# Optimization experiments

Measured on AMD Instinct MI355X. Metric: run time of the kernel, lower is better.

## Reference

```python
import jax, jax.numpy as jnp
import numpy as np

EPS = 1e-5

def setup_inputs() -> dict:
    key = jax.random.key(0)
    ks = jax.random.split(key, 10)
    B, N, D = 1, 20000, 256
    E, H = 320000, 8
    s = 1.0 / np.sqrt(D)
    return {
        "node_embeddings": jax.random.normal(ks[0], (B, N, D), jnp.float32),
        "edge_index": jax.random.randint(ks[1], (2, E), 0, N, jnp.int32),
        "edge_weights": jax.random.uniform(ks[2], (E,), jnp.float32),
        "Wq": jax.random.normal(ks[3], (D, D), jnp.float32) * s,
        "Wk": jax.random.normal(ks[4], (D, D), jnp.float32) * s,
        "Wv": jax.random.normal(ks[5], (D, D), jnp.float32) * s,
        "We": jax.random.normal(ks[6], (H,), jnp.float32),  # edge_encoder weight [num_heads,1] squeezed
        "Wo": jax.random.normal(ks[7], (D, D), jnp.float32) * s,
        "ln_g": jnp.ones((D,), jnp.float32),
        "ln_b": jnp.zeros((D,), jnp.float32),
    }

def reference(node_embeddings, edge_index, edge_weights, Wq, Wk, Wv, We, Wo, ln_g, ln_b):
    B, N, D = node_embeddings.shape
    H = We.shape[0]
    hd = D // H
    scale = 1.0 / np.sqrt(hd)
    residual = node_embeddings

    # projections -> [B, N, H, hd]
    Q = (node_embeddings @ Wq).reshape(B, N, H, hd)
    K = (node_embeddings @ Wk).reshape(B, N, H, hd)
    V = (node_embeddings @ Wv).reshape(B, N, H, hd)

    src = edge_index[0]
    tgt = edge_index[1]
    E = src.shape[0]

    # gather per edge, edge axis leading for segment ops: [E, B, H, hd]
    Q_e = jnp.moveaxis(Q[:, src], 1, 0)
    K_e = jnp.moveaxis(K[:, tgt], 1, 0)
    V_e = jnp.moveaxis(V[:, tgt], 1, 0)

    # per-edge scores [E, B, H]
    scores = (Q_e * K_e).sum(-1) * scale
    bias = edge_weights[:, None] * We[None, :]            # [E, H]
    scores = scores + bias[:, None, :]

    # scatter softmax grouped by source node
    m = jax.ops.segment_max(scores, src, num_segments=N)   # [N, B, H]
    p = jnp.exp(scores - m[src])
    denom = jax.ops.segment_sum(p, src, num_segments=N)    # [N, B, H]
    attn = p / denom[src]                                   # [E, B, H]

    # scatter-add weighted V -> [N, B, H, hd]
    weighted = attn[..., None] * V_e
    agg = jax.ops.segment_sum(weighted.reshape(E, -1), src, num_segments=N)
    agg = agg.reshape(N, B, H, hd)

    attn_out = jnp.moveaxis(agg, 0, 1).reshape(B, N, D)     # [B, N, D]
    out = attn_out @ Wo

    x = out + residual
    mu = x.mean(-1, keepdims=True)
    var = ((x - mu) ** 2).mean(-1, keepdims=True)
    return (x - mu) / jnp.sqrt(var + EPS) * ln_g + ln_b
```

## Files before the change

kernel.cpp:

```cpp
#include <hip/hip_runtime.h>
#include <hip/hip_bf16.h>

typedef __attribute__((ext_vector_type(8))) short short8;
typedef __attribute__((ext_vector_type(4))) short short4_t;
typedef __attribute__((ext_vector_type(4))) float f32x4;

#define CH 64

__device__ __forceinline__ ushort f2b(float f) {
  __hip_bfloat16 h = __float2bfloat16(f);
  return *reinterpret_cast<ushort*>(&h);
}
__device__ __forceinline__ float b2f(ushort u) {
  return __uint_as_float(((unsigned)u) << 16);
}
__device__ __forceinline__ void wave_lds_sync() {
  asm volatile("s_waitcnt lgkmcnt(0)" ::: "memory");
  __builtin_amdgcn_wave_barrier();
}

__global__ __launch_bounds__(256) void pre_kernel(
    const float* __restrict__ X, ushort* __restrict__ Xb, int nX,
    const float* __restrict__ Wq, const float* __restrict__ Wk,
    const float* __restrict__ Wv, const float* __restrict__ Wo,
    ushort* __restrict__ Wt, int* __restrict__ counts, int N, int nxb) {
  __shared__ float L[32][33];
  int b = blockIdx.x;
  int t = threadIdx.x;
  if (b < nxb) {
    int i = (b * 256 + t) * 8;
    if (i >= nX) return;
    float4 x0 = *reinterpret_cast<const float4*>(X + i);
    float4 x1 = *reinterpret_cast<const float4*>(X + i + 4);
    short8 o;
    o[0] = (short)f2b(x0.x); o[1] = (short)f2b(x0.y);
    o[2] = (short)f2b(x0.z); o[3] = (short)f2b(x0.w);
    o[4] = (short)f2b(x1.x); o[5] = (short)f2b(x1.y);
    o[6] = (short)f2b(x1.z); o[7] = (short)f2b(x1.w);
    *reinterpret_cast<short8*>(Xb + i) = o;
  } else if (b < nxb + 256) {
    int bx = b - nxb;
    int mat = bx >> 6;
    int tile = bx & 63;
    int tr = (tile >> 3) * 32;
    int tc = (tile & 7) * 32;
    const float* W = (mat == 0) ? Wq : (mat == 1) ? Wk : (mat == 2) ? Wv : Wo;
    int c = t & 31, r8 = t >> 5;
#pragma unroll
    for (int rr = 0; rr < 4; ++rr) {
      int r = r8 + rr * 8;
      L[r][c] = W[(size_t)(tr + r) * 256 + tc + c];
    }
    __syncthreads();
#pragma unroll
    for (int rr = 0; rr < 4; ++rr) {
      int cc = r8 + rr * 8;
      Wt[(size_t)(mat * 256 + tc + cc) * 256 + tr + c] = f2b(L[c][cc]);
    }
  } else {
    int i = (b - nxb - 256) * 256 + t;
    if (i < N) counts[i] = 0;
  }
}

__global__ __launch_bounds__(256) void hist_gemm(
    const ushort* __restrict__ Xb, const ushort* __restrict__ Wt,
    ushort* __restrict__ QKVb, const int* __restrict__ src,
    int* __restrict__ counts, int N, int E, int ngemm) {
  __shared__ ushort sA[128 * 64];
  __shared__ ushort sB[128 * 64];
  int bid = blockIdx.x;
  int t = threadIdx.x;
  if (bid >= ngemm) {
    int e = (bid - ngemm) * 256 + t;
    if (e < E) atomicAdd(&counts[src[e]], 1);
    return;
  }
  int bx = bid / 6, by = bid % 6;
  char* cA = (char*)sA;
  char* cB = (char*)sB;
  int lane = t & 63, w = t >> 6;
  int wr = w >> 1, wc = w & 1;
  int row0 = bx * 128;
  int lr = lane & 15, kg = lane >> 4;
  f32x4 acc[4][4] = {};
  for (int k0 = 0; k0 < 256; k0 += 64) {
#pragma unroll
    for (int it = 0; it < 4; ++it) {
      int slot = t + it * 256;
      int row = slot >> 3, kc = slot & 7;
      int grow = min(row0 + row, N - 1);
      short8 va = *reinterpret_cast<const short8*>(Xb + (size_t)grow * 256 + k0 + kc * 8);
      *reinterpret_cast<short8*>(cA + ((row * 128 + kc * 16) ^ ((row & 7) << 4))) = va;
      short8 vb = *reinterpret_cast<const short8*>(Wt + (size_t)(by * 128 + row) * 256 + k0 + kc * 8);
      *reinterpret_cast<short8*>(cB + ((row * 128 + kc * 16) ^ ((row & 7) << 4))) = vb;
    }
    __syncthreads();
#pragma unroll
    for (int ks = 0; ks < 2; ++ks) {
      short8 af[4], bf[4];
#pragma unroll
      for (int fr = 0; fr < 4; ++fr) {
        int row = wr * 64 + fr * 16 + lr;
        af[fr] = *reinterpret_cast<const short8*>(
            cA + ((row * 128 + ks * 64 + kg * 16) ^ ((row & 7) << 4)));
      }
#pragma unroll
      for (int fc = 0; fc < 4; ++fc) {
        int col = wc * 64 + fc * 16 + lr;
        bf[fc] = *reinterpret_cast<const short8*>(
            cB + ((col * 128 + ks * 64 + kg * 16) ^ ((col & 7) << 4)));
      }
#pragma unroll
      for (int fr = 0; fr < 4; ++fr)
#pragma unroll
        for (int fc = 0; fc < 4; ++fc)
          acc[fr][fc] = __builtin_amdgcn_mfma_f32_16x16x32_bf16(af[fr], bf[fc], acc[fr][fc], 0, 0, 0);
    }
    __syncthreads();
  }
  int orow = kg * 4;
#pragma unroll
  for (int fr = 0; fr < 4; ++fr)
#pragma unroll
    for (int fc = 0; fc < 4; ++fc)
#pragma unroll
      for (int r = 0; r < 4; ++r) {
        int row = row0 + wr * 64 + fr * 16 + orow + r;
        int col = by * 128 + wc * 64 + fc * 16 + lr;
        if (row < N) QKVb[(size_t)row * 768 + col] = f2b(acc[fr][fc][r]);
      }
}

__global__ __launch_bounds__(1024) void scan_kernel(
    const int* __restrict__ counts, int* __restrict__ offs, int* __restrict__ cursor, int N) {
  __shared__ int wsum[16];
  __shared__ int wexc[16];
  __shared__ int s_total;
  int t = threadIdx.x;
  int lane = t & 63, wv = t >> 6;
  int per = (N + 1023) >> 10;
  int b0 = t * per;
  int e0 = min(b0 + per, N);
  int sum = 0;
  for (int i = b0; i < e0; ++i) sum += counts[i];
  int x = sum;
#pragma unroll
  for (int off = 1; off < 64; off <<= 1) {
    int y = __shfl_up(x, off);
    if (lane >= off) x += y;
  }
  if (lane == 63) wsum[wv] = x;
  __syncthreads();
  if (t < 64) {
    int s = (lane < 16) ? wsum[lane] : 0;
    int xs = s;
#pragma unroll
    for (int off = 1; off < 16; off <<= 1) {
      int y = __shfl_up(xs, off);
      if (lane >= off) xs += y;
    }
    if (lane < 16) wexc[lane] = xs - s;
    if (lane == 15) s_total = xs;
  }
  __syncthreads();
  int running = wexc[wv] + (x - sum);
  for (int i = b0; i < e0; ++i) {
    int c = counts[i];
    offs[i] = running;
    cursor[i] = running;
    running += c;
  }
  if (t == 0) offs[N] = s_total;
}

__global__ void scatter_kernel(const int* __restrict__ src, const int* __restrict__ tgt,
                               const float* __restrict__ ew, int* __restrict__ cursor,
                               int* __restrict__ tgt_s, float* __restrict__ w_s, int E) {
  int e = blockIdx.x * blockDim.x + threadIdx.x;
  if (e < E) {
    int pos = atomicAdd(&cursor[src[e]], 1);
    tgt_s[pos] = tgt[e];
    w_s[pos] = ew[e];
  }
}

__global__ __launch_bounds__(256) void attn_kernel(
    const ushort* __restrict__ QKVb,
    const int* __restrict__ offs, const int* __restrict__ tgt_s, const float* __restrict__ w_s,
    const float* __restrict__ We, ushort* __restrict__ AGGb, int N) {
  __shared__ float s_p[4][CH][8];
  __shared__ int s_tgt[4][CH];
  __shared__ float s_w[4][CH];
  int t = threadIdx.x;
  int w = t >> 6;
  int l = t & 63;
  int i = blockIdx.x * 4 + w;
  if (i >= N) return;
  int e8 = l >> 3;
  int h = l & 7;
  int hacc = l >> 3;
  const float scale = 0.17677669529663687f;
  float we = We[h];

  float qf[32];
  {
    const short8* qr = reinterpret_cast<const short8*>(QKVb + (size_t)i * 768 + h * 32);
#pragma unroll
    for (int d = 0; d < 4; ++d) {
      short8 qv = qr[d];
#pragma unroll
      for (int x = 0; x < 8; ++x) qf[d * 8 + x] = b2f((ushort)qv[x]);
    }
  }

  float m = -1e30f, lsum = 0.f;
  float acc0 = 0.f, acc1 = 0.f, acc2 = 0.f, acc3 = 0.f;
  int beg = offs[i], end = offs[i + 1];

  for (int base = beg; base < end; base += CH) {
    int cnt = min(CH, end - base);
    int cnt_pad = (cnt + 7) & ~7;
    {
      bool valid = l < cnt;
      int tg = valid ? tgt_s[base + l] : i;
      float ww = valid ? w_s[base + l] : 0.f;
      s_tgt[w][l] = tg;
      s_w[w][l] = ww;
    }
    wave_lds_sync();

    short8 kc[4], kn[4];
    {
      const short8* p = reinterpret_cast<const short8*>(
          QKVb + (size_t)s_tgt[w][e8] * 768 + 256 + h * 32);
#pragma unroll
      for (int d = 0; d < 4; ++d) kc[d] = p[d];
    }
    if (8 < cnt_pad) {
      const short8* p = reinterpret_cast<const short8*>(
          QKVb + (size_t)s_tgt[w][8 + e8] * 768 + 256 + h * 32);
#pragma unroll
      for (int d = 0; d < 4; ++d) kn[d] = p[d];
    }
    short4_t vc[8], vn[8];
#pragma unroll
    for (int k = 0; k < 8; ++k)
      vc[k] = *reinterpret_cast<const short4_t*>(
          QKVb + (size_t)s_tgt[w][k] * 768 + 512 + l * 4);
    if (8 < cnt_pad) {
#pragma unroll
      for (int k = 0; k < 8; ++k)
        vn[k] = *reinterpret_cast<const short4_t*>(
            QKVb + (size_t)s_tgt[w][8 + k] * 768 + 512 + l * 4);
    }

    float s_local[8];
#pragma unroll
    for (int it = 0; it < 8; ++it) s_local[it] = -1e30f;
    float cmax = -1e30f;
#pragma unroll
    for (int it = 0; it < 8; ++it) {
      if (it * 8 >= cnt_pad) break;
      float dot = 0.f;
#pragma unroll
      for (int d = 0; d < 4; ++d)
#pragma unroll
        for (int x = 0; x < 8; ++x)
          dot += qf[d * 8 + x] * b2f((ushort)kc[d][x]);
      int j = it * 8 + e8;
      float s = (j < cnt) ? dot * scale + s_w[w][j] * we : -1e30f;
      s_local[it] = s;
      cmax = fmaxf(cmax, s);
#pragma unroll
      for (int d = 0; d < 4; ++d) kc[d] = kn[d];
      if ((it + 2) * 8 < cnt_pad) {
        const short8* p = reinterpret_cast<const short8*>(
            QKVb + (size_t)s_tgt[w][(it + 2) * 8 + e8] * 768 + 256 + h * 32);
#pragma unroll
        for (int d = 0; d < 4; ++d) kn[d] = p[d];
      }
    }
    cmax = fmaxf(cmax, __shfl_xor(cmax, 8));
    cmax = fmaxf(cmax, __shfl_xor(cmax, 16));
    cmax = fmaxf(cmax, __shfl_xor(cmax, 32));
    float newm = fmaxf(m, cmax);
    float f = __expf(m - newm);
    float psum = 0.f;
#pragma unroll
    for (int it = 0; it < 8; ++it) {
      if (it * 8 >= cnt_pad) break;
      int j = it * 8 + e8;
      float p = __expf(s_local[it] - newm);
      s_p[w][j][h] = p;
      psum += p;
    }
    psum += __shfl_xor(psum, 8);
    psum += __shfl_xor(psum, 16);
    psum += __shfl_xor(psum, 32);
    lsum = lsum * f + psum;
    m = newm;
    float f_acc = __shfl(f, hacc);
    acc0 *= f_acc; acc1 *= f_acc; acc2 *= f_acc; acc3 *= f_acc;
    wave_lds_sync();

#pragma unroll
    for (int g = 0; g < 8; ++g) {
      if (g * 8 >= cnt_pad) break;
      float pv[8];
#pragma unroll
      for (int k = 0; k < 8; ++k) pv[k] = s_p[w][g * 8 + k][hacc];
#pragma unroll
      for (int k = 0; k < 8; ++k) {
        acc0 += pv[k] * b2f((ushort)vc[k][0]);
        acc1 += pv[k] * b2f((ushort)vc[k][1]);
        acc2 += pv[k] * b2f((ushort)vc[k][2]);
        acc3 += pv[k] * b2f((ushort)vc[k][3]);
      }
#pragma unroll
      for (int k = 0; k < 8; ++k) vc[k] = vn[k];
      if ((g + 2) * 8 < cnt_pad) {
#pragma unroll
        for (int k = 0; k < 8; ++k)
          vn[k] = *reinterpret_cast<const short4_t*>(
              QKVb + (size_t)s_tgt[w][(g + 2) * 8 + k] * 768 + 512 + l * 4);
      }
    }
    wave_lds_sync();
  }
  float lsum_acc = __shfl(lsum, hacc);
  float rinv = (lsum_acc > 0.f) ? 1.f / lsum_acc : 0.f;
  short4_t o;
  o[0] = (short)f2b(acc0 * rinv);
  o[1] = (short)f2b(acc1 * rinv);
  o[2] = (short)f2b(acc2 * rinv);
  o[3] = (short)f2b(acc3 * rinv);
  *reinterpret_cast<short4_t*>(AGGb + (size_t)i * 256 + l * 4) = o;
}

__global__ __launch_bounds__(256) void out_ln(
    const ushort* __restrict__ AGGb, const ushort* __restrict__ Wot,
    const float* __restrict__ X, const float* __restrict__ g, const float* __restrict__ bb,
    float* __restrict__ out, int N) {
  __shared__ ushort sA[64 * 64];
  __shared__ ushort sB[256 * 64];
  char* cA = (char*)sA;
  char* cB = (char*)sB;
  int t = threadIdx.x;
  int lane = t & 63, w = t >> 6;
  int row0 = blockIdx.x * 64;
  int lr = lane & 15, kg = lane >> 4;
  f32x4 acc[16] = {};
  for (int k0 = 0; k0 < 256; k0 += 64) {
#pragma unroll
    for (int it = 0; it < 2; ++it) {
      int slot = t + it * 256;
      int row = slot >> 3, kc = slot & 7;
      int grow = min(row0 + row, N - 1);
      short8 va = *reinterpret_cast<const short8*>(AGGb + (size_t)grow * 256 + k0 + kc * 8);
      *reinterpret_cast<short8*>(cA + ((row * 128 + kc * 16) ^ ((row & 7) << 4))) = va;
    }
#pragma unroll
    for (int it = 0; it < 8; ++it) {
      int slot = t + it * 256;
      int col = slot >> 3, kc = slot & 7;
      short8 vb = *reinterpret_cast<const short8*>(Wot + (size_t)col * 256 + k0 + kc * 8);
      *reinterpret_cast<short8*>(cB + ((col * 128 + kc * 16) ^ ((col & 7) << 4))) = vb;
    }
    __syncthreads();
#pragma unroll
    for (int ks = 0; ks < 2; ++ks) {
      int arow = w * 16 + lr;
      short8 a = *reinterpret_cast<const short8*>(
          cA + ((arow * 128 + ks * 64 + kg * 16) ^ ((arow & 7) << 4)));
#pragma unroll
      for (int fc = 0; fc < 16; ++fc) {
        int col = fc * 16 + lr;
        short8 b = *reinterpret_cast<const short8*>(
            cB + ((col * 128 + ks * 64 + kg * 16) ^ ((col & 7) << 4)));
        acc[fc] = __builtin_amdgcn_mfma_f32_16x16x32_bf16(a, b, acc[fc], 0, 0, 0);
      }
    }
    __syncthreads();
  }
  float g16[16], b16[16];
#pragma unroll
  for (int fc = 0; fc < 16; ++fc) {
    g16[fc] = g[fc * 16 + lr];
    b16[fc] = bb[fc * 16 + lr];
  }
#pragma unroll
  for (int r = 0; r < 4; ++r) {
    int rowl = kg * 4 + r;
    int grow = row0 + w * 16 + rowl;
    int growc = min(grow, N - 1);
    float xv[16];
    float s = 0.f, ss = 0.f;
#pragma unroll
    for (int fc = 0; fc < 16; ++fc) {
      float v = acc[fc][r] + X[(size_t)growc * 256 + fc * 16 + lr];
      xv[fc] = v;
      s += v;
      ss += v * v;
    }
    s += __shfl_xor(s, 1);  ss += __shfl_xor(ss, 1);
    s += __shfl_xor(s, 2);  ss += __shfl_xor(ss, 2);
    s += __shfl_xor(s, 4);  ss += __shfl_xor(ss, 4);
    s += __shfl_xor(s, 8);  ss += __shfl_xor(ss, 8);
    float mu = s * (1.f / 256.f);
    float var = ss * (1.f / 256.f) - mu * mu;
    float rs = rsqrtf(var + 1e-5f);
    if (grow < N) {
#pragma unroll
      for (int fc = 0; fc < 16; ++fc)
        out[(size_t)grow * 256 + fc * 16 + lr] = (xv[fc] - mu) * rs * g16[fc] + b16[fc];
    }
  }
}

extern "C" void kernel_launch(void* const* d_in, const int* in_sizes, int n_in,
                              void* d_out, int out_size, void* d_ws, size_t ws_size,
                              hipStream_t stream) {
  const float* X  = (const float*)d_in[0];
  const int* eidx = (const int*)d_in[1];
  const float* ew = (const float*)d_in[2];
  const float* Wq = (const float*)d_in[3];
  const float* Wk = (const float*)d_in[4];
  const float* Wv = (const float*)d_in[5];
  const float* We = (const float*)d_in[6];
  const float* Wo = (const float*)d_in[7];
  const float* g  = (const float*)d_in[8];
  const float* b  = (const float*)d_in[9];
  int N = in_sizes[0] / 256;
  int E = in_sizes[1] / 2;
  const int* src = eidx;
  const int* tgt = eidx + E;
  float* out = (float*)d_out;

  char* w = (char*)d_ws;
  ushort* Xb   = (ushort*)w;  w += (size_t)N * 256 * 2;
  ushort* Wt   = (ushort*)w;  w += (size_t)1024 * 256 * 2;
  ushort* QKVb = (ushort*)w;  w += (size_t)N * 768 * 2;
  ushort* AGGb = (ushort*)w;  w += (size_t)N * 256 * 2;
  int* counts  = (int*)w;     w += (size_t)N * 4;
  int* offs    = (int*)w;     w += (size_t)(N + 1) * 4;
  int* cursor  = (int*)w;     w += (size_t)N * 4;
  int* tgt_s   = (int*)w;     w += (size_t)E * 4;
  float* w_s   = (float*)w;   w += (size_t)E * 4;
  const ushort* Wot = Wt + (size_t)768 * 256;

  int nX = N * 256;
  int nxb = (nX / 8 + 255) / 256;
  int nzero = (N + 255) / 256;
  pre_kernel<<<nxb + 256 + nzero, 256, 0, stream>>>(X, Xb, nX, Wq, Wk, Wv, Wo, Wt, counts, N, nxb);

  int ngemm = ((N + 127) / 128) * 6;
  int nhist = (E + 255) / 256;
  hist_gemm<<<ngemm + nhist, 256, 0, stream>>>(Xb, Wt, QKVb, src, counts, N, E, ngemm);

  scan_kernel<<<1, 1024, 0, stream>>>(counts, offs, cursor, N);
  scatter_kernel<<<(E + 255) / 256, 256, 0, stream>>>(src, tgt, ew, cursor, tgt_s, w_s, E);
  attn_kernel<<<(N + 3) / 4, 256, 0, stream>>>(QKVb, offs, tgt_s, w_s, We, AGGb, N);
  out_ln<<<(N + 63) / 64, 256, 0, stream>>>(AGGb, Wot, X, g, b, out, N);
}
```

Baseline: 167.1 us.

## Fuse X bf16 conversion into QKV GEMM; defer V loads and raise wave priority

Removes the separate X-to-bf16 conversion pass and its intermediate buffer: the QKV GEMM now loads fp32 X directly and converts while staging into shared memory. This saves a full write and read of the bf16 copy, but the GEMM reads twice the bytes for A and repeats the conversion once per column block (6 times). In the attention kernel, V loads are moved after the score loop to cut register pressure during the K phase. The per-chunk work is also wrapped in s_setprio to raise wave priority.

```diff
diff --git a/kernel.cpp b/kernel.cpp
--- a/kernel.cpp
+++ b/kernel.cpp
@@ -20,28 +20,15 @@
 }
 
 __global__ __launch_bounds__(256) void pre_kernel(
-    const float* __restrict__ X, ushort* __restrict__ Xb, int nX,
     const float* __restrict__ Wq, const float* __restrict__ Wk,
     const float* __restrict__ Wv, const float* __restrict__ Wo,
-    ushort* __restrict__ Wt, int* __restrict__ counts, int N, int nxb) {
+    ushort* __restrict__ Wt, int* __restrict__ counts, int N) {
   __shared__ float L[32][33];
   int b = blockIdx.x;
   int t = threadIdx.x;
-  if (b < nxb) {
-    int i = (b * 256 + t) * 8;
-    if (i >= nX) return;
-    float4 x0 = *reinterpret_cast<const float4*>(X + i);
-    float4 x1 = *reinterpret_cast<const float4*>(X + i + 4);
-    short8 o;
-    o[0] = (short)f2b(x0.x); o[1] = (short)f2b(x0.y);
-    o[2] = (short)f2b(x0.z); o[3] = (short)f2b(x0.w);
-    o[4] = (short)f2b(x1.x); o[5] = (short)f2b(x1.y);
-    o[6] = (short)f2b(x1.z); o[7] = (short)f2b(x1.w);
-    *reinterpret_cast<short8*>(Xb + i) = o;
-  } else if (b < nxb + 256) {
-    int bx = b - nxb;
-    int mat = bx >> 6;
-    int tile = bx & 63;
+  if (b < 256) {
+    int mat = b >> 6;
+    int tile = b & 63;
     int tr = (tile >> 3) * 32;
     int tc = (tile & 7) * 32;
     const float* W = (mat == 0) ? Wq : (mat == 1) ? Wk : (mat == 2) ? Wv : Wo;
@@ -58,13 +45,13 @@
       Wt[(size_t)(mat * 256 + tc + cc) * 256 + tr + c] = f2b(L[c][cc]);
     }
   } else {
-    int i = (b - nxb - 256) * 256 + t;
+    int i = (b - 256) * 256 + t;
     if (i < N) counts[i] = 0;
   }
 }
 
 __global__ __launch_bounds__(256) void hist_gemm(
-    const ushort* __restrict__ Xb, const ushort* __restrict__ Wt,
+    const float* __restrict__ X, const ushort* __restrict__ Wt,
     ushort* __restrict__ QKVb, const int* __restrict__ src,
     int* __restrict__ counts, int N, int E, int ngemm) {
   __shared__ ushort sA[128 * 64];
@@ -90,7 +77,14 @@
       int slot = t + it * 256;
       int row = slot >> 3, kc = slot & 7;
       int grow = min(row0 + row, N - 1);
-      short8 va = *reinterpret_cast<const short8*>(Xb + (size_t)grow * 256 + k0 + kc * 8);
+      const float* xp = X + (size_t)grow * 256 + k0 + kc * 8;
+      float4 x0 = *reinterpret_cast<const float4*>(xp);
+      float4 x1 = *reinterpret_cast<const float4*>(xp + 4);
+      short8 va;
+      va[0] = (short)f2b(x0.x); va[1] = (short)f2b(x0.y);
+      va[2] = (short)f2b(x0.z); va[3] = (short)f2b(x0.w);
+      va[4] = (short)f2b(x1.x); va[5] = (short)f2b(x1.y);
+      va[6] = (short)f2b(x1.z); va[7] = (short)f2b(x1.w);
       *reinterpret_cast<short8*>(cA + ((row * 128 + kc * 16) ^ ((row & 7) << 4))) = va;
       short8 vb = *reinterpret_cast<const short8*>(Wt + (size_t)(by * 128 + row) * 256 + k0 + kc * 8);
       *reinterpret_cast<short8*>(cB + ((row * 128 + kc * 16) ^ ((row & 7) << 4))) = vb;
@@ -230,6 +224,7 @@
     }
     wave_lds_sync();
 
+    __builtin_amdgcn_s_setprio(1);
     short8 kc[4], kn[4];
     {
       const short8* p = reinterpret_cast<const short8*>(
@@ -242,17 +237,6 @@
           QKVb + (size_t)s_tgt[w][8 + e8] * 768 + 256 + h * 32);
 #pragma unroll
       for (int d = 0; d < 4; ++d) kn[d] = p[d];
-    }
-    short4_t vc[8], vn[8];
-#pragma unroll
-    for (int k = 0; k < 8; ++k)
-      vc[k] = *reinterpret_cast<const short4_t*>(
-          QKVb + (size_t)s_tgt[w][k] * 768 + 512 + l * 4);
-    if (8 < cnt_pad) {
-#pragma unroll
-      for (int k = 0; k < 8; ++k)
-        vn[k] = *reinterpret_cast<const short4_t*>(
-            QKVb + (size_t)s_tgt[w][8 + k] * 768 + 512 + l * 4);
     }
 
     float s_local[8];
@@ -281,6 +265,19 @@
         for (int d = 0; d < 4; ++d) kn[d] = p[d];
       }
     }
+
+    short4_t vc[8], vn[8];
+#pragma unroll
+    for (int k = 0; k < 8; ++k)
+      vc[k] = *reinterpret_cast<const short4_t*>(
+          QKVb + (size_t)s_tgt[w][k] * 768 + 512 + l * 4);
+    if (8 < cnt_pad) {
+#pragma unroll
+      for (int k = 0; k < 8; ++k)
+        vn[k] = *reinterpret_cast<const short4_t*>(
+            QKVb + (size_t)s_tgt[w][8 + k] * 768 + 512 + l * 4);
+    }
+
     cmax = fmaxf(cmax, __shfl_xor(cmax, 8));
     cmax = fmaxf(cmax, __shfl_xor(cmax, 16));
     cmax = fmaxf(cmax, __shfl_xor(cmax, 32));
@@ -326,6 +323,7 @@
               QKVb + (size_t)s_tgt[w][(g + 2) * 8 + k] * 768 + 512 + l * 4);
       }
     }
+    __builtin_amdgcn_s_setprio(0);
     wave_lds_sync();
   }
   float lsum_acc = __shfl(lsum, hacc);
@@ -438,7 +436,6 @@
   float* out = (float*)d_out;
 
   char* w = (char*)d_ws;
-  ushort* Xb   = (ushort*)w;  w += (size_t)N * 256 * 2;
   ushort* Wt   = (ushort*)w;  w += (size_t)1024 * 256 * 2;
   ushort* QKVb = (ushort*)w;  w += (size_t)N * 768 * 2;
   ushort* AGGb = (ushort*)w;  w += (size_t)N * 256 * 2;
@@ -449,14 +446,12 @@
   float* w_s   = (float*)w;   w += (size_t)E * 4;
   const ushort* Wot = Wt + (size_t)768 * 256;
 
-  int nX = N * 256;
-  int nxb = (nX / 8 + 255) / 256;
   int nzero = (N + 255) / 256;
-  pre_kernel<<<nxb + 256 + nzero, 256, 0, stream>>>(X, Xb, nX, Wq, Wk, Wv, Wo, Wt, counts, N, nxb);
+  pre_kernel<<<256 + nzero, 256, 0, stream>>>(Wq, Wk, Wv, Wo, Wt, counts, N);
 
   int ngemm = ((N + 127) / 128) * 6;
   int nhist = (E + 255) / 256;
-  hist_gemm<<<ngemm + nhist, 256, 0, stream>>>(Xb, Wt, QKVb, src, counts, N, E, ngemm);
+  hist_gemm<<<ngemm + nhist, 256, 0, stream>>>(X, Wt, QKVb, src, counts, N, E, ngemm);
 
   scan_kernel<<<1, 1024, 0, stream>>>(counts, offs, cursor, N);
   scatter_kernel<<<(E + 255) / 256, 256, 0, stream>>>(src, tgt, ew, cursor, tgt_s, w_s, E);
```

After: 169.7 us. No clear change (+1.6%).

## Store K and V in FP8 and pack edge target/weight into int2

Applied to the files above, without the earlier changes.

The QKV projection now writes Q as bf16 and K and V as FP8 e4m3 in separate buffers. This halves the bytes the attention kernel gathers per edge for keys and values. The scatter step packs each edge's target and weight into one int2, and the GEMM block index is remapped across XCDs for locality. The V prefetch double-buffering is dropped in favour of direct loads, and FP8 quantization of K/V adds precision loss.

```diff
diff --git a/kernel.cpp b/kernel.cpp
--- a/kernel.cpp
+++ b/kernel.cpp
@@ -1,8 +1,9 @@
 #include <hip/hip_runtime.h>
 #include <hip/hip_bf16.h>
+#include <hip/hip_fp8.h>
 
 typedef __attribute__((ext_vector_type(8))) short short8;
-typedef __attribute__((ext_vector_type(4))) short short4_t;
+typedef __attribute__((ext_vector_type(16))) unsigned char uchar16;
 typedef __attribute__((ext_vector_type(4))) float f32x4;
 
 #define CH 64
@@ -13,6 +14,15 @@
 }
 __device__ __forceinline__ float b2f(ushort u) {
   return __uint_as_float(((unsigned)u) << 16);
+}
+__device__ __forceinline__ unsigned char f2e4(float f) {
+  __hip_fp8_e4m3 h(f);
+  return *reinterpret_cast<unsigned char*>(&h);
+}
+__device__ __forceinline__ float e42f(unsigned char u) {
+  __hip_fp8_e4m3 h;
+  *reinterpret_cast<unsigned char*>(&h) = u;
+  return (float)h;
 }
 __device__ __forceinline__ void wave_lds_sync() {
   asm volatile("s_waitcnt lgkmcnt(0)" ::: "memory");
@@ -63,9 +73,10 @@
   }
 }
 
-__global__ __launch_bounds__(256) void hist_gemm(
+__global__ __launch_bounds__(256) void gemm_hist(
     const ushort* __restrict__ Xb, const ushort* __restrict__ Wt,
-    ushort* __restrict__ QKVb, const int* __restrict__ src,
+    ushort* __restrict__ Qb, unsigned char* __restrict__ Kb8,
+    unsigned char* __restrict__ Vb8, const int* __restrict__ src,
     int* __restrict__ counts, int N, int E, int ngemm) {
   __shared__ ushort sA[128 * 64];
   __shared__ ushort sB[128 * 64];
@@ -76,7 +87,10 @@
     if (e < E) atomicAdd(&counts[src[e]], 1);
     return;
   }
-  int bx = bid / 6, by = bid % 6;
+  int q = ngemm >> 3, r = ngemm & 7;
+  int xcd = bid & 7;
+  int wgid = (xcd < r ? xcd * (q + 1) : r * (q + 1) + (xcd - r) * q) + (bid >> 3);
+  int bx = wgid / 6, by = wgid % 6;
   char* cA = (char*)sA;
   char* cB = (char*)sB;
   int lane = t & 63, w = t >> 6;
@@ -120,15 +134,21 @@
     __syncthreads();
   }
   int orow = kg * 4;
+  int mat = by >> 1;
 #pragma unroll
   for (int fr = 0; fr < 4; ++fr)
 #pragma unroll
     for (int fc = 0; fc < 4; ++fc)
 #pragma unroll
-      for (int r = 0; r < 4; ++r) {
-        int row = row0 + wr * 64 + fr * 16 + orow + r;
-        int col = by * 128 + wc * 64 + fc * 16 + lr;
-        if (row < N) QKVb[(size_t)row * 768 + col] = f2b(acc[fr][fc][r]);
+      for (int r2 = 0; r2 < 4; ++r2) {
+        int row = row0 + wr * 64 + fr * 16 + orow + r2;
+        int col = (by & 1) * 128 + wc * 64 + fc * 16 + lr;
+        if (row < N) {
+          float v = acc[fr][fc][r2];
+          if (mat == 0)      Qb[(size_t)row * 256 + col]  = f2b(v);
+          else if (mat == 1) Kb8[(size_t)row * 256 + col] = f2e4(v);
+          else               Vb8[(size_t)row * 256 + col] = f2e4(v);
+        }
       }
 }
 
@@ -176,18 +196,18 @@
 
 __global__ void scatter_kernel(const int* __restrict__ src, const int* __restrict__ tgt,
                                const float* __restrict__ ew, int* __restrict__ cursor,
-                               int* __restrict__ tgt_s, float* __restrict__ w_s, int E) {
+                               int2* __restrict__ ews, int E) {
   int e = blockIdx.x * blockDim.x + threadIdx.x;
   if (e < E) {
     int pos = atomicAdd(&cursor[src[e]], 1);
-    tgt_s[pos] = tgt[e];
-    w_s[pos] = ew[e];
+    ews[pos] = make_int2(tgt[e], __float_as_int(ew[e]));
   }
 }
 
 __global__ __launch_bounds__(256) void attn_kernel(
-    const ushort* __restrict__ QKVb,
-    const int* __restrict__ offs, const int* __restrict__ tgt_s, const float* __restrict__ w_s,
+    const ushort* __restrict__ Qb, const unsigned char* __restrict__ Kb8,
+    const unsigned char* __restrict__ Vb8,
+    const int* __restrict__ offs, const int2* __restrict__ ews,
     const float* __restrict__ We, ushort* __restrict__ AGGb, int N) {
   __shared__ float s_p[4][CH][8];
   __shared__ int s_tgt[4][CH];
@@ -205,7 +225,7 @@
 
   float qf[32];
   {
-    const short8* qr = reinterpret_cast<const short8*>(QKVb + (size_t)i * 768 + h * 32);
+    const short8* qr = reinterpret_cast<const short8*>(Qb + (size_t)i * 256 + h * 32);
 #pragma unroll
     for (int d = 0; d < 4; ++d) {
       short8 qv = qr[d];
@@ -223,62 +243,46 @@
     int cnt_pad = (cnt + 7) & ~7;
     {
       bool valid = l < cnt;
-      int tg = valid ? tgt_s[base + l] : i;
-      float ww = valid ? w_s[base + l] : 0.f;
-      s_tgt[w][l] = tg;
-      s_w[w][l] = ww;
+      int2 te = valid ? ews[base + l] : make_int2(i, 0);
+      s_tgt[w][l] = te.x;
+      s_w[w][l] = valid ? __int_as_float(te.y) : 0.f;
     }
     wave_lds_sync();
 
-    short8 kc[4], kn[4];
+    float s_local[8];
+#pragma unroll
+    for (int it = 0; it < 8; ++it) s_local[it] = -1e30f;
+
+    uchar16 kc[2], kn[2];
     {
-      const short8* p = reinterpret_cast<const short8*>(
-          QKVb + (size_t)s_tgt[w][e8] * 768 + 256 + h * 32);
-#pragma unroll
-      for (int d = 0; d < 4; ++d) kc[d] = p[d];
+      const uchar16* p = reinterpret_cast<const uchar16*>(
+          Kb8 + (size_t)s_tgt[w][e8] * 256 + h * 32);
+      kc[0] = p[0]; kc[1] = p[1];
     }
     if (8 < cnt_pad) {
-      const short8* p = reinterpret_cast<const short8*>(
-          QKVb + (size_t)s_tgt[w][8 + e8] * 768 + 256 + h * 32);
-#pragma unroll
-      for (int d = 0; d < 4; ++d) kn[d] = p[d];
-    }
-    short4_t vc[8], vn[8];
-#pragma unroll
-    for (int k = 0; k < 8; ++k)
-      vc[k] = *reinterpret_cast<const short4_t*>(
-          QKVb + (size_t)s_tgt[w][k] * 768 + 512 + l * 4);
-    if (8 < cnt_pad) {
-#pragma unroll
-      for (int k = 0; k < 8; ++k)
-        vn[k] = *reinterpret_cast<const short4_t*>(
-            QKVb + (size_t)s_tgt[w][8 + k] * 768 + 512 + l * 4);
-    }
-
-    float s_local[8];
-#pragma unroll
-    for (int it = 0; it < 8; ++it) s_local[it] = -1e30f;
+      const uchar16* p = reinterpret_cast<const uchar16*>(
+          Kb8 + (size_t)s_tgt[w][8 + e8] * 256 + h * 32);
+      kn[0] = p[0]; kn[1] = p[1];
+    }
     float cmax = -1e30f;
 #pragma unroll
     for (int it = 0; it < 8; ++it) {
       if (it * 8 >= cnt_pad) break;
       float dot = 0.f;
 #pragma unroll
-      for (int d = 0; d < 4; ++d)
-#pragma unroll
-        for (int x = 0; x < 8; ++x)
-          dot += qf[d * 8 + x] * b2f((ushort)kc[d][x]);
+      for (int c = 0; c < 2; ++c)
+#pragma unroll
+        for (int x = 0; x < 16; ++x)
+          dot += qf[c * 16 + x] * e42f(kc[c][x]);
       int j = it * 8 + e8;
       float s = (j < cnt) ? dot * scale + s_w[w][j] * we : -1e30f;
       s_local[it] = s;
       cmax = fmaxf(cmax, s);
-#pragma unroll
-      for (int d = 0; d < 4; ++d) kc[d] = kn[d];
+      kc[0] = kn[0]; kc[1] = kn[1];
       if ((it + 2) * 8 < cnt_pad) {
-        const short8* p = reinterpret_cast<const short8*>(
-            QKVb + (size_t)s_tgt[w][(it + 2) * 8 + e8] * 768 + 256 + h * 32);
-#pragma unroll
-        for (int d = 0; d < 4; ++d) kn[d] = p[d];
+        const uchar16* p = reinterpret_cast<const uchar16*>(
+            Kb8 + (size_t)s_tgt[w][(it + 2) * 8 + e8] * 256 + h * 32);
+        kn[0] = p[0]; kn[1] = p[1];
       }
     }
     cmax = fmaxf(cmax, __shfl_xor(cmax, 8));
@@ -308,34 +312,32 @@
     for (int g = 0; g < 8; ++g) {
       if (g * 8 >= cnt_pad) break;
       float pv[8];
-#pragma unroll
-      for (int k = 0; k < 8; ++k) pv[k] = s_p[w][g * 8 + k][hacc];
+      unsigned vv[8];
 #pragma unroll
       for (int k = 0; k < 8; ++k) {
-        acc0 += pv[k] * b2f((ushort)vc[k][0]);
-        acc1 += pv[k] * b2f((ushort)vc[k][1]);
-        acc2 += pv[k] * b2f((ushort)vc[k][2]);
-        acc3 += pv[k] * b2f((ushort)vc[k][3]);
-      }
-#pragma unroll
-      for (int k = 0; k < 8; ++k) vc[k] = vn[k];
-      if ((g + 2) * 8 < cnt_pad) {
-#pragma unroll
-        for (int k = 0; k < 8; ++k)
-          vn[k] = *reinterpret_cast<const short4_t*>(
-              QKVb + (size_t)s_tgt[w][(g + 2) * 8 + k] * 768 + 512 + l * 4);
+        int j = g * 8 + k;
+        pv[k] = s_p[w][j][hacc];
+        vv[k] = *reinterpret_cast<const unsigned*>(
+            Vb8 + (size_t)s_tgt[w][j] * 256 + l * 4);
+      }
+#pragma unroll
+      for (int k = 0; k < 8; ++k) {
+        acc0 += pv[k] * e42f((unsigned char)(vv[k] & 0xff));
+        acc1 += pv[k] * e42f((unsigned char)((vv[k] >> 8) & 0xff));
+        acc2 += pv[k] * e42f((unsigned char)((vv[k] >> 16) & 0xff));
+        acc3 += pv[k] * e42f((unsigned char)(vv[k] >> 24));
       }
     }
     wave_lds_sync();
   }
   float lsum_acc = __shfl(lsum, hacc);
   float rinv = (lsum_acc > 0.f) ? 1.f / lsum_acc : 0.f;
-  short4_t o;
-  o[0] = (short)f2b(acc0 * rinv);
-  o[1] = (short)f2b(acc1 * rinv);
-  o[2] = (short)f2b(acc2 * rinv);
-  o[3] = (short)f2b(acc3 * rinv);
-  *reinterpret_cast<short4_t*>(AGGb + (size_t)i * 256 + l * 4) = o;
+  ushort o0 = f2b(acc0 * rinv), o1 = f2b(acc1 * rinv);
+  ushort o2 = f2b(acc2 * rinv), o3 = f2b(acc3 * rinv);
+  short8 dummy;
+  ushort4 o = make_ushort4(o0, o1, o2, o3);
+  *reinterpret_cast<ushort4*>(AGGb + (size_t)i * 256 + l * 4) = o;
+  (void)dummy;
 }
 
 __global__ __launch_bounds__(256) void out_ln(
@@ -438,15 +440,16 @@
   float* out = (float*)d_out;
 
   char* w = (char*)d_ws;
-  ushort* Xb   = (ushort*)w;  w += (size_t)N * 256 * 2;
-  ushort* Wt   = (ushort*)w;  w += (size_t)1024 * 256 * 2;
-  ushort* QKVb = (ushort*)w;  w += (size_t)N * 768 * 2;
-  ushort* AGGb = (ushort*)w;  w += (size_t)N * 256 * 2;
-  int* counts  = (int*)w;     w += (size_t)N * 4;
-  int* offs    = (int*)w;     w += (size_t)(N + 1) * 4;
-  int* cursor  = (int*)w;     w += (size_t)N * 4;
-  int* tgt_s   = (int*)w;     w += (size_t)E * 4;
-  float* w_s   = (float*)w;   w += (size_t)E * 4;
+  ushort* Xb   = (ushort*)w;        w += (size_t)N * 256 * 2;
+  ushort* Wt   = (ushort*)w;        w += (size_t)1024 * 256 * 2;
+  ushort* Qb   = (ushort*)w;        w += (size_t)N * 256 * 2;
+  unsigned char* Kb8 = (unsigned char*)w;  w += (size_t)N * 256;
+  unsigned char* Vb8 = (unsigned char*)w;  w += (size_t)N * 256;
+  ushort* AGGb = (ushort*)w;        w += (size_t)N * 256 * 2;
+  int* counts  = (int*)w;           w += (size_t)N * 4;
+  int* offs    = (int*)w;           w += (size_t)(N + 1) * 4;
+  int* cursor  = (int*)w;           w += (size_t)N * 4;
+  int2* ews    = (int2*)w;          w += (size_t)E * 8;
   const ushort* Wot = Wt + (size_t)768 * 256;
 
   int nX = N * 256;
@@ -456,10 +459,10 @@
 
   int ngemm = ((N + 127) / 128) * 6;
   int nhist = (E + 255) / 256;
-  hist_gemm<<<ngemm + nhist, 256, 0, stream>>>(Xb, Wt, QKVb, src, counts, N, E, ngemm);
+  gemm_hist<<<ngemm + nhist, 256, 0, stream>>>(Xb, Wt, Qb, Kb8, Vb8, src, counts, N, E, ngemm);
 
   scan_kernel<<<1, 1024, 0, stream>>>(counts, offs, cursor, N);
-  scatter_kernel<<<(E + 255) / 256, 256, 0, stream>>>(src, tgt, ew, cursor, tgt_s, w_s, E);
-  attn_kernel<<<(N + 3) / 4, 256, 0, stream>>>(QKVb, offs, tgt_s, w_s, We, AGGb, N);
+  scatter_kernel<<<(E + 255) / 256, 256, 0, stream>>>(src, tgt, ew, cursor, ews, E);
+  attn_kernel<<<(N + 3) / 4, 256, 0, stream>>>(Qb, Kb8, Vb8, offs, ews, We, AGGb, N);
   out_ln<<<(N + 63) / 64, 256, 0, stream>>>(AGGb, Wot, X, g, b, out, N);
 }
```

Result: faster. 154.5 us (-7.5%).
